# Optimization experiments

Hardware: AMD Instinct MI355X
Metric: run time of the kernel (lower is better)

## Reference

```python
import jax, jax.numpy as jnp
import numpy as np

DIM = 32
DEPTH = 2  # closed-form Lyndon-basis log-signature implemented for depth 2


def setup_inputs() -> dict:
    key = jax.random.key(0)
    B, L, D = 512, 2048, DIM
    x = jax.random.normal(key, (B, L, D), dtype=jnp.float32)
    return {"x": x}


def _logsig_depth2(x):
    # x: (B, L, D) batch of paths.
    dx = x[:, 1:, :] - x[:, :-1, :]                     # (B, L-1, D) increments
    prefix = jnp.cumsum(dx, axis=1)                      # inclusive prefix sums
    level1 = prefix[:, -1, :]                            # (B, D) total displacement
    prefix_excl = prefix - dx                            # prefix up to t-1 (exclusive)
    # level-2 signature S_ij = sum_t prefix_excl[t, i] * dx[t, j]  -> (B, D, D)
    S2 = jnp.einsum("bli,blj->bij", prefix_excl, dx)
    # log-signature level 2 = antisymmetric part (Levy areas), Lyndon words i<j
    A = 0.5 * (S2 - jnp.swapaxes(S2, 1, 2))             # (B, D, D)
    iu, ju = jnp.triu_indices(x.shape[-1], k=1)          # row-major upper triangle
    areas = A[:, iu, ju]                                 # (B, D*(D-1)/2)
    return jnp.concatenate([level1, areas], axis=-1)     # (B, D + D*(D-1)/2)


def reference(x):
    # Faithful batched equivalent of iisignature.logsig(path, prepare(dim, 2))
    # for every path in the batch (Lyndon basis, depth 2).
    return _logsig_depth2(x)
```

## Files before the change

### kernel.cpp

```cpp
#include <hip/hip_runtime.h>
#include <stdint.h>


constexpr int kB   = 512;
constexpr int kL   = 2048;
constexpr int kD   = 32;
constexpr int kOut = 528;
constexpr int kTw  = 256;
constexpr int kPan = 32;
constexpr int kNP  = kTw / kPan;

typedef __attribute__((ext_vector_type(8))) short bfrag;
typedef __attribute__((ext_vector_type(4))) float f4acc;
union FragU { uint32_t u[4]; bfrag f; };

__global__ __launch_bounds__(256, 4)
void logsig_mfma(const float* __restrict__ x, float* __restrict__ out) {
    __shared__ float sM[kD * kD];
    __shared__ float sx0[kD], sL1[kD];

    const int b     = blockIdx.x >> 1;
    const int halfc = blockIdx.x & 1;
    const int tid   = threadIdx.x;
    const int wave  = tid >> 6;
    const int lane  = tid & 63;
    const int m     = lane & 15;
    const int q     = lane >> 4;

    const float* __restrict__ xb = x + (size_t)b * (kL * kD);
    const int t0 = (halfc * 4 + wave) * kTw;
    const int rb0 = t0 + q * 8;

    const uint32_t* __restrict__ base =
        (const uint32_t*)xb + (size_t)rb0 * kD + m;

    f4acc acc[4];
    #pragma unroll
    for (int t = 0; t < 4; ++t)
        #pragma unroll
        for (int e = 0; e < 4; ++e) acc[t][e] = 0.0f;

    auto load_panel = [&](int p, uint32_t* e0, uint32_t* e1) {
        const uint32_t* bp = base + (size_t)p * kPan * kD;
        #pragma unroll
        for (int j = 0; j < 8; ++j) {
            e0[j] = bp[j * kD];
            e1[j] = bp[j * kD + 16];
        }
        const int rb = rb0 + p * kPan;
        const int ex = (rb + 8 <= kL - 1 ? 8 : (kL - 1) - rb) * kD;
        e0[8] = bp[ex];
        e1[8] = bp[ex + 16];
    };

    auto make_frags = [&](const uint32_t* e, FragU& AH, FragU& AL,
                          FragU& BH, FragU& BL) {
        uint32_t l[9];
        #pragma unroll
        for (int j = 0; j < 9; ++j) {
            const uint32_t fh = e[j] & 0xffff0000u;
            const float r = __builtin_bit_cast(float, e[j])
                          - __builtin_bit_cast(float, fh);
            l[j] = __builtin_bit_cast(uint32_t, r);
        }
        #pragma unroll
        for (int d = 0; d < 4; ++d) {
            AH.u[d] = __builtin_amdgcn_perm(e[2*d+1], e[2*d],   0x07060302u);
            AL.u[d] = __builtin_amdgcn_perm(l[2*d+1], l[2*d],   0x07060302u);
            BH.u[d] = __builtin_amdgcn_perm(e[2*d+2], e[2*d+1], 0x07060302u);
            BL.u[d] = __builtin_amdgcn_perm(l[2*d+2], l[2*d+1], 0x07060302u);
        }
    };

    uint32_t cur0[9], cur1[9], nxt0[9], nxt1[9];
    load_panel(0, cur0, cur1);

    #pragma unroll
    for (int p = 0; p < kNP; ++p) {
        if (p + 1 < kNP) load_panel(p + 1, nxt0, nxt1);

        FragU A0H, A0L, B0H, B0L, A1H, A1L, B1H, B1L;
        make_frags(cur0, A0H, A0L, B0H, B0L);
        make_frags(cur1, A1H, A1L, B1H, B1L);

        acc[0] = __builtin_amdgcn_mfma_f32_16x16x32_bf16(A0H.f, B0H.f, acc[0], 0, 0, 0);
        acc[0] = __builtin_amdgcn_mfma_f32_16x16x32_bf16(A0H.f, B0L.f, acc[0], 0, 0, 0);
        acc[0] = __builtin_amdgcn_mfma_f32_16x16x32_bf16(A0L.f, B0H.f, acc[0], 0, 0, 0);
        acc[1] = __builtin_amdgcn_mfma_f32_16x16x32_bf16(A0H.f, B1H.f, acc[1], 0, 0, 0);
        acc[1] = __builtin_amdgcn_mfma_f32_16x16x32_bf16(A0H.f, B1L.f, acc[1], 0, 0, 0);
        acc[1] = __builtin_amdgcn_mfma_f32_16x16x32_bf16(A0L.f, B1H.f, acc[1], 0, 0, 0);
        acc[2] = __builtin_amdgcn_mfma_f32_16x16x32_bf16(A1H.f, B0H.f, acc[2], 0, 0, 0);
        acc[2] = __builtin_amdgcn_mfma_f32_16x16x32_bf16(A1H.f, B0L.f, acc[2], 0, 0, 0);
        acc[2] = __builtin_amdgcn_mfma_f32_16x16x32_bf16(A1L.f, B0H.f, acc[2], 0, 0, 0);
        acc[3] = __builtin_amdgcn_mfma_f32_16x16x32_bf16(A1H.f, B1H.f, acc[3], 0, 0, 0);
        acc[3] = __builtin_amdgcn_mfma_f32_16x16x32_bf16(A1H.f, B1L.f, acc[3], 0, 0, 0);
        acc[3] = __builtin_amdgcn_mfma_f32_16x16x32_bf16(A1L.f, B1H.f, acc[3], 0, 0, 0);

        #pragma unroll
        for (int j = 0; j < 9; ++j) { cur0[j] = nxt0[j]; cur1[j] = nxt1[j]; }
    }

    for (int c = tid; c < kD * kD; c += 256) sM[c] = 0.0f;
    if (tid < kD) {
        const float x0v = xb[tid];
        const float xev = xb[(size_t)(kL - 1) * kD + tid];
        sx0[tid] = x0v;
        sL1[tid] = xev - x0v;
    }
    __syncthreads();

    #pragma unroll
    for (int t = 0; t < 4; ++t) {
        const int tr = t >> 1, tc = t & 1;
        #pragma unroll
        for (int e = 0; e < 4; ++e) {
            const int row = 16 * tr + q * 4 + e;
            const int col = 16 * tc + m;
            atomicAdd(&sM[row * kD + col], acc[t][e]);
        }
    }
    __syncthreads();

    float* ob = out + (size_t)b * kOut;
    for (int o = tid; o < kOut; o += 256) {
        if (o < 32) {
            if (halfc == 0) ob[o] = sL1[o];
        } else {
            int p = o - 32, i = 0;
            while (p >= 31 - i) { p -= 31 - i; ++i; }
            const int j = i + 1 + p;
            float v = 0.5f * (sM[i * kD + j] - sM[j * kD + i]);
            if (halfc == 0)
                v += 0.5f * (sx0[j] * sL1[i] - sx0[i] * sL1[j]);
            atomicAdd(ob + o, v);
        }
    }
}

extern "C" void kernel_launch(void* const* d_in, const int* in_sizes, int n_in,
                              void* d_out, int out_size, void* d_ws, size_t ws_size,
                              hipStream_t stream) {
    const float* x = (const float*)d_in[0];
    float* out = (float*)d_out;
    hipMemsetAsync(out, 0, (size_t)out_size * sizeof(float), stream);
    logsig_mfma<<<dim3(kB * 2), dim3(256), 0, stream>>>(x, out);
}
```

Before: 208.6 us.

## Use one block per path, reduce waves in shared memory, drop memset and atomics

Each path is now handled by a single block whose four waves each cover 512 time steps, where before two blocks each covered half the path. Per-wave accumulators go to separate shared-memory slabs and are summed deterministically, replacing LDS atomics. Output is written directly, which removes the global atomics and the separate memset launch. In exchange the grid shrinks to 512 blocks, so there is less parallelism to hide memory latency on a GPU with many CUs. The panel loop also moves to a ping-pong register buffer with partial unrolling.

```diff
diff --git a/kernel.cpp b/kernel.cpp
--- a/kernel.cpp
+++ b/kernel.cpp
@@ -6,7 +6,7 @@
 constexpr int kL   = 2048;
 constexpr int kD   = 32;
 constexpr int kOut = 528;
-constexpr int kTw  = 256;
+constexpr int kTw  = 512;
 constexpr int kPan = 32;
 constexpr int kNP  = kTw / kPan;
 
@@ -14,21 +14,21 @@
 typedef __attribute__((ext_vector_type(4))) float f4acc;
 union FragU { uint32_t u[4]; bfrag f; };
 
-__global__ __launch_bounds__(256, 4)
+__global__ __launch_bounds__(256, 2)
 void logsig_mfma(const float* __restrict__ x, float* __restrict__ out) {
+    __shared__ float sW[4][kD * kD];
     __shared__ float sM[kD * kD];
     __shared__ float sx0[kD], sL1[kD];
 
-    const int b     = blockIdx.x >> 1;
-    const int halfc = blockIdx.x & 1;
-    const int tid   = threadIdx.x;
-    const int wave  = tid >> 6;
-    const int lane  = tid & 63;
-    const int m     = lane & 15;
-    const int q     = lane >> 4;
+    const int b    = blockIdx.x;
+    const int tid  = threadIdx.x;
+    const int wave = tid >> 6;
+    const int lane = tid & 63;
+    const int m    = lane & 15;
+    const int q    = lane >> 4;
 
     const float* __restrict__ xb = x + (size_t)b * (kL * kD);
-    const int t0 = (halfc * 4 + wave) * kTw;
+    const int t0  = wave * kTw;
     const int rb0 = t0 + q * 8;
 
     const uint32_t* __restrict__ base =
@@ -72,16 +72,17 @@
         }
     };
 
-    uint32_t cur0[9], cur1[9], nxt0[9], nxt1[9];
-    load_panel(0, cur0, cur1);
+    uint32_t buf[2][2][9];
+    load_panel(0, buf[0][0], buf[0][1]);
 
-    #pragma unroll
+    #pragma unroll 2
     for (int p = 0; p < kNP; ++p) {
-        if (p + 1 < kNP) load_panel(p + 1, nxt0, nxt1);
+        const int cu = p & 1, nx = cu ^ 1;
+        if (p + 1 < kNP) load_panel(p + 1, buf[nx][0], buf[nx][1]);
 
         FragU A0H, A0L, B0H, B0L, A1H, A1L, B1H, B1L;
-        make_frags(cur0, A0H, A0L, B0H, B0L);
-        make_frags(cur1, A1H, A1L, B1H, B1L);
+        make_frags(buf[cu][0], A0H, A0L, B0H, B0L);
+        make_frags(buf[cu][1], A1H, A1L, B1H, B1L);
 
         acc[0] = __builtin_amdgcn_mfma_f32_16x16x32_bf16(A0H.f, B0H.f, acc[0], 0, 0, 0);
         acc[0] = __builtin_amdgcn_mfma_f32_16x16x32_bf16(A0H.f, B0L.f, acc[0], 0, 0, 0);
@@ -95,12 +96,18 @@
         acc[3] = __builtin_amdgcn_mfma_f32_16x16x32_bf16(A1H.f, B1H.f, acc[3], 0, 0, 0);
         acc[3] = __builtin_amdgcn_mfma_f32_16x16x32_bf16(A1H.f, B1L.f, acc[3], 0, 0, 0);
         acc[3] = __builtin_amdgcn_mfma_f32_16x16x32_bf16(A1L.f, B1H.f, acc[3], 0, 0, 0);
-
-        #pragma unroll
-        for (int j = 0; j < 9; ++j) { cur0[j] = nxt0[j]; cur1[j] = nxt1[j]; }
     }
 
-    for (int c = tid; c < kD * kD; c += 256) sM[c] = 0.0f;
+    #pragma unroll
+    for (int t = 0; t < 4; ++t) {
+        const int tr = t >> 1, tc = t & 1;
+        #pragma unroll
+        for (int e = 0; e < 4; ++e) {
+            const int row = 16 * tr + q * 4 + e;
+            const int col = 16 * tc + m;
+            sW[wave][row * kD + col] = acc[t][e];
+        }
+    }
     if (tid < kD) {
         const float x0v = xb[tid];
         const float xev = xb[(size_t)(kL - 1) * kD + tid];
@@ -109,30 +116,20 @@
     }
     __syncthreads();
 
-    #pragma unroll
-    for (int t = 0; t < 4; ++t) {
-        const int tr = t >> 1, tc = t & 1;
-        #pragma unroll
-        for (int e = 0; e < 4; ++e) {
-            const int row = 16 * tr + q * 4 + e;
-            const int col = 16 * tc + m;
-            atomicAdd(&sM[row * kD + col], acc[t][e]);
-        }
-    }
+    for (int c = tid; c < kD * kD; c += 256)
+        sM[c] = sW[0][c] + sW[1][c] + sW[2][c] + sW[3][c];
     __syncthreads();
 
     float* ob = out + (size_t)b * kOut;
     for (int o = tid; o < kOut; o += 256) {
         if (o < 32) {
-            if (halfc == 0) ob[o] = sL1[o];
+            ob[o] = sL1[o];
         } else {
             int p = o - 32, i = 0;
             while (p >= 31 - i) { p -= 31 - i; ++i; }
             const int j = i + 1 + p;
-            float v = 0.5f * (sM[i * kD + j] - sM[j * kD + i]);
-            if (halfc == 0)
-                v += 0.5f * (sx0[j] * sL1[i] - sx0[i] * sL1[j]);
-            atomicAdd(ob + o, v);
+            ob[o] = 0.5f * (sM[i * kD + j] - sM[j * kD + i]
+                            + sx0[j] * sL1[i] - sx0[i] * sL1[j]);
         }
     }
 }
@@ -142,6 +139,5 @@
                               hipStream_t stream) {
     const float* x = (const float*)d_in[0];
     float* out = (float*)d_out;
-    hipMemsetAsync(out, 0, (size_t)out_size * sizeof(float), stream);
-    logsig_mfma<<<dim3(kB * 2), dim3(256), 0, stream>>>(x, out);
+    logsig_mfma<<<dim3(kB), dim3(256), 0, stream>>>(x, out);
 }
```

After: 191.6 us. -8.1%, faster.
